# Performance work log

Hardware: AMD Instinct MI355X
Metric: run time of the kernel (lower is better)

Reference implementation:

```python
import jax, jax.numpy as jnp
import numpy as np

B, L, E, H, ENC, V, NL = 64, 512, 128, 512, 256, 4, 2
SOS = 4


def setup_inputs() -> dict:
    key = jax.random.key(0)
    ks = jax.random.split(key, 20)
    s = 0.05
    r = lambda k, shp: (jax.random.normal(k, shp, jnp.float32) * s)
    return {
        "encoder_outputs": jax.random.normal(ks[0], (B, L, ENC), jnp.float32),
        "targets": jax.random.randint(ks[1], (B, L), 0, V),
        "encoder_mask": jnp.ones((B, L), bool),
        "teacher_forcing_ratio": 1,
        "emb": r(ks[2], (V + 2, E)),
        "Wh": r(ks[3], (H, H)),
        "Ws": r(ks[4], (H, ENC)),
        "v": r(ks[5], (1, H)),
        "Wih0": r(ks[6], (3 * H, E + ENC)),
        "Whh0": r(ks[7], (3 * H, H)),
        "bih0": r(ks[8], (3 * H,)),
        "bhh0": r(ks[9], (3 * H,)),
        "Wih1": r(ks[10], (3 * H, H)),
        "Whh1": r(ks[11], (3 * H, H)),
        "bih1": r(ks[12], (3 * H,)),
        "bhh1": r(ks[13], (3 * H,)),
        "Wout": r(ks[14], (V, H)),
        "bout": r(ks[15], (V,)),
        "Winit": r(ks[16], (H * NL, ENC)),
        "binit": r(ks[17], (H * NL,)),
    }


def gru_cell(x, h, Wih, Whh, bih, bhh):
    # PyTorch GRUCell math
    gi = x @ Wih.T + bih
    gh = h @ Whh.T + bhh
    ir, iz, inn = jnp.split(gi, 3, axis=-1)
    hr, hz, hn = jnp.split(gh, 3, axis=-1)
    rg = jax.nn.sigmoid(ir + hr)
    zg = jax.nn.sigmoid(iz + hz)
    ng = jnp.tanh(inn + rg * hn)
    return (1.0 - zg) * ng + zg * h


def reference(encoder_outputs, targets, encoder_mask, teacher_forcing_ratio,
              emb, Wh, Ws, v, Wih0, Whh0, bih0, bhh0, Wih1, Whh1, bih1, bhh1,
              Wout, bout, Winit, binit):
    # init hidden: masked mean-pool -> linear -> tanh, (NL, B, H)
    maskf = encoder_mask[..., None].astype(jnp.float32)
    pooled = (encoder_outputs * maskf).sum(1) / jnp.clip(maskf.sum(1), 1.0)
    h0 = jnp.tanh((pooled @ Winit.T + binit).reshape(B, NL, H).transpose(1, 0, 2))

    # attention keys precomputed once (same linear applied each step in torch)
    keys = jnp.einsum('ble,he->blh', encoder_outputs, Ws)  # (B, L, H)

    # teacher forcing ratio fixed at 1 -> inputs known ahead of time
    tokens = jnp.concatenate([jnp.full((B, 1), SOS, targets.dtype), targets[:, :-1]], axis=1)
    emb_seq = emb[tokens]  # (B, L, E)

    neg = jnp.finfo(jnp.float32).min

    def step(h, e_t):
        q = h[-1] @ Wh.T                                   # (B, H)
        energy = jnp.tanh(q[:, None, :] + keys)            # (B, L, H)
        scores = jnp.einsum('blh,h->bl', energy, v[0])     # (B, L)
        scores = jnp.where(encoder_mask, scores, neg)
        attn = jax.nn.softmax(scores, axis=-1)
        ctx = jnp.einsum('bl,ble->be', attn, encoder_outputs)
        x = jnp.concatenate([e_t, ctx], axis=-1)           # (B, E+ENC)
        h0n = gru_cell(x, h[0], Wih0, Whh0, bih0, bhh0)
        h1n = gru_cell(h0n, h[1], Wih1, Whh1, bih1, bhh1)
        logits = h1n @ Wout.T + bout                       # (B, V)
        return jnp.stack([h0n, h1n]), logits

    _, logits = jax.lax.scan(step, h0, emb_seq.transpose(1, 0, 2))
    return logits.transpose(1, 0, 2)  # (B, L, V)
```

## Files before the change

kernel.cpp:

```cpp
#include <hip/hip_runtime.h>
#include <cstdint>
#include <cstddef>


#define BB   64
#define LL   512
#define EE   128
#define HH   512
#define ED   256
#define VV   4
#define SOS  4

#define NBLK 256
#define NTHR 512

typedef unsigned short ushort8 __attribute__((ext_vector_type(8)));
typedef unsigned int uint;

static const size_t OFF_KEYS = 0;
static const size_t OFF_WH   = 33554432;
static const size_t OFF_WHH0 = 34078720;
static const size_t OFF_WIH1 = 35651584;
static const size_t OFF_WHH1 = 37224448;
static const size_t OFF_WIHC = 38797312;
static const size_t OFF_GTOK = 39583744;
static const size_t OFF_H0   = 39620608;
static const size_t OFF_H1   = 39751680;
static const size_t OFF_QQ   = 39882752;
static const size_t OFF_CTXP = 40407040;
static const size_t OFF_SS   = 40669184;
static const size_t OFF_H0Q  = 40670208;
static const size_t OFF_H1Q  = 40801280;
static const size_t OFF_FLG  = 40932352;
static const size_t OFF_CNT  = 40948736;
static const size_t OFF_LP   = 40949248;

#define L_KEYS 0
#define L_H0F  131072
#define L_H1F  133120
#define L_Q    135168
#define L_VV   137344
#define L_CTX  139520
#define L_SCB  140544
#define L_ATB  141056
#define L_CT   141568
#define L_RED  142592
#define L_PRED 142656
#define L_GH0  154944
#define L_GH1  156480
#define L_TOT  158016

__device__ __forceinline__ int qidx(int h) { return h + ((h >> 7) << 3); }

__device__ __forceinline__ float bfu(unsigned short u) {
  return __uint_as_float(((unsigned)u) << 16);
}
__device__ __forceinline__ float bflo(uint u) { return __uint_as_float(u << 16); }
__device__ __forceinline__ float bfhi(uint u) { return __uint_as_float(u & 0xffff0000u); }
__device__ __forceinline__ unsigned short f2bf(float f) {
  unsigned u = __float_as_uint(f);
  unsigned r = 0x7FFFu + ((u >> 16) & 1u);
  return (unsigned short)((u + r) >> 16);
}
__device__ __forceinline__ float tanh_fast(float x) {
  x = __builtin_amdgcn_fmed3f(x, -10.f, 10.f);
  float t = __builtin_amdgcn_exp2f(x * 2.8853900817779268f);
  return (t - 1.f) * __builtin_amdgcn_rcpf(t + 1.f);
}
__device__ __forceinline__ float sigmoid_fast(float x) {
  x = __builtin_amdgcn_fmed3f(x, -30.f, 30.f);
  float t = __builtin_amdgcn_exp2f(x * -1.4426950408889634f);
  return __builtin_amdgcn_rcpf(1.f + t);
}
__device__ __forceinline__ float exp_fast(float x) {
  return __builtin_amdgcn_exp2f(x * 1.4426950408889634f);
}
__device__ __forceinline__ float gloadf(const float* p) {
  return __hip_atomic_load(p, __ATOMIC_RELAXED, __HIP_MEMORY_SCOPE_AGENT);
}
__device__ __forceinline__ void gstoref(float* p, float v) {
  __hip_atomic_store(p, v, __ATOMIC_RELAXED, __HIP_MEMORY_SCOPE_AGENT);
}
__device__ __forceinline__ uint gloadu(const uint* p) {
  return __hip_atomic_load(p, __ATOMIC_RELAXED, __HIP_MEMORY_SCOPE_AGENT);
}
__device__ __forceinline__ void gstoreu(uint* p, uint v) {
  __hip_atomic_store(p, v, __ATOMIC_RELAXED, __HIP_MEMORY_SCOPE_AGENT);
}

__device__ __forceinline__ void quad_sync(char* ws, int b, int j, uint gen) {
  asm volatile("s_waitcnt vmcnt(0)" ::: "memory");
  __syncthreads();
  if (threadIdx.x == 0) {
    uint* fl = (uint*)(ws + OFF_FLG);
    gstoreu(fl + (size_t)(b * 4 + j) * 16, gen);
    #pragma unroll
    for (int p = 0; p < 4; ++p) {
      if (p == j) continue;
      while (gloadu(fl + (size_t)(b * 4 + p) * 16) < gen)
        __builtin_amdgcn_s_sleep(4);
    }
  }
  __syncthreads();
}


__global__ void k_prep(const float* Wh, const float* Whh0, const float* Wih0,
                       const float* Wih1, const float* Whh1, char* ws) {
  unsigned short* Whbf   = (unsigned short*)(ws + OFF_WH);
  unsigned short* Whh0bf = (unsigned short*)(ws + OFF_WHH0);
  unsigned short* Wih1bf = (unsigned short*)(ws + OFF_WIH1);
  unsigned short* Whh1bf = (unsigned short*)(ws + OFF_WHH1);
  unsigned short* WihCbf = (unsigned short*)(ws + OFF_WIHC);
  const int tot = 262144 + 786432 * 3 + 393216;
  for (int i = blockIdx.x * blockDim.x + threadIdx.x; i < tot; i += gridDim.x * blockDim.x) {
    if (i < 262144) { Whbf[i] = f2bf(Wh[i]); }
    else if (i < 262144 + 786432) { int jj = i - 262144; Whh0bf[jj] = f2bf(Whh0[jj]); }
    else if (i < 262144 + 2 * 786432) { int jj = i - 262144 - 786432; Wih1bf[jj] = f2bf(Wih1[jj]); }
    else if (i < 262144 + 3 * 786432) { int jj = i - 262144 - 2 * 786432; Whh1bf[jj] = f2bf(Whh1[jj]); }
    else {
      int jj = i - 262144 - 3 * 786432;
      int r = jj >> 8, e = jj & 255;
      WihCbf[jj] = f2bf(Wih0[(size_t)r * 384 + 128 + e]);
    }
  }
}

__global__ void k_gitok(const float* emb, const float* Wih0, const float* bih0, char* ws) {
  float* gt = (float*)(ws + OFF_GTOK);
  const int vt = blockIdx.x;
  const int tid = threadIdx.x;
  __shared__ float ev[EE];
  if (tid < EE) ev[tid] = emb[(size_t)vt * EE + tid];
  __syncthreads();
  for (int r = tid; r < 1536; r += 256) {
    float a = bih0[r];
    const float* wr = Wih0 + (size_t)r * 384;
    for (int e = 0; e < EE; ++e) a += wr[e] * ev[e];
    gt[(size_t)vt * 1536 + r] = a;
  }
}

__global__ void k_keys(const float* enc, const float* Ws, char* ws) {
  unsigned short* keys = (unsigned short*)(ws + OFF_KEYS);
  __shared__ float et[32][ED];
  const int tid = threadIdx.x;
  const int row0 = blockIdx.x * 32;
  for (int r = 0; r < 32; ++r) et[r][tid] = enc[(size_t)(row0 + r) * ED + tid];
  __syncthreads();
  for (int hhh = 0; hhh < 2; ++hhh) {
    const int h = hhh * 256 + tid;
    float acc[32];
    #pragma unroll
    for (int ll = 0; ll < 32; ++ll) acc[ll] = 0.f;
    const float4* wrow = (const float4*)(Ws + (size_t)h * ED);
    for (int e4 = 0; e4 < 64; ++e4) {
      float4 w = wrow[e4];
      #pragma unroll
      for (int ll = 0; ll < 32; ++ll) {
        acc[ll] += w.x * et[ll][e4 * 4] + w.y * et[ll][e4 * 4 + 1]
                 + w.z * et[ll][e4 * 4 + 2] + w.w * et[ll][e4 * 4 + 3];
      }
    }
    for (int ll = 0; ll < 32; ++ll)
      keys[(size_t)(row0 + ll) * HH + h] = f2bf(acc[ll]);
  }
}

__global__ void k_init(const float* enc, const float* Winit, const float* binit, char* ws) {
  const int b = blockIdx.x;
  const int tid = threadIdx.x;
  __shared__ float pooled[ED];
  float acc = 0.f;
  for (int l = 0; l < LL; ++l) acc += enc[((size_t)b * LL + l) * ED + tid];
  pooled[tid] = acc * (1.0f / 512.0f);
  __syncthreads();
  float* h0 = (float*)(ws + OFF_H0);
  float* h1 = (float*)(ws + OFF_H1);
  for (int pass = 0; pass < 4; ++pass) {
    const int jj = pass * 256 + tid;
    float a = binit[jj];
    const float* wr = Winit + (size_t)jj * ED;
    for (int e = 0; e < ED; ++e) a += wr[e] * pooled[e];
    const float val = tanh_fast(a);
    const int nl = jj >> 9, h = jj & 511;
    if (nl == 0) h0[(size_t)b * HH + h] = val;
    else h1[(size_t)b * HH + h] = val;
  }
  if (b == 0) {
    uint* fl = (uint*)(ws + OFF_FLG);
    for (int i = tid; i < 4096; i += 256) fl[i] = 0u;
    uint* cnt = (uint*)(ws + OFF_CNT);
    if (tid < 128) cnt[tid] = 0u;
  }
}

__launch_bounds__(NTHR, 1)
__global__ void k_decode(char* ws, const float* enc, const int* targets,
                         const float* vvec, const float* bhh0, const float* bhh1,
                         const float* bih1, const float* Wout) {
  extern __shared__ char smem[];
  const int tid = threadIdx.x;

  __shared__ int roleSh[2];
  if (tid == 0) {
    uint xcd;
    asm volatile("s_getreg_b32 %0, hwreg(HW_REG_XCC_ID)" : "=s"(xcd));
    xcd &= 7u;
    uint* cnt = (uint*)(ws + OFF_CNT);
    uint rank = __hip_atomic_fetch_add(cnt + (size_t)xcd * 16, 1u,
                                       __ATOMIC_RELAXED, __HIP_MEMORY_SCOPE_AGENT);
    roleSh[0] = (int)((((xcd >> 2) * 32) + rank) & 63);
    roleSh[1] = (int)(xcd & 3);
  }
  __syncthreads();
  const int b = roleSh[0], j = roleSh[1];

  const unsigned short* keysg  = (const unsigned short*)(ws + OFF_KEYS);
  const unsigned short* Whbf   = (const unsigned short*)(ws + OFF_WH);
  const unsigned short* Whh0bf = (const unsigned short*)(ws + OFF_WHH0);
  const unsigned short* Wih1bf = (const unsigned short*)(ws + OFF_WIH1);
  const unsigned short* Whh1bf = (const unsigned short*)(ws + OFF_WHH1);
  const unsigned short* WihCbf = (const unsigned short*)(ws + OFF_WIHC);
  const float* gi_tok = (const float*)(ws + OFF_GTOK);

  float* QQgf   = (float*)(ws + OFF_QQ)   + (size_t)b * 2048;
  float* CTXPgf = (float*)(ws + OFF_CTXP) + (size_t)b * 1024;
  float* SSg    = (float*)(ws + OFF_SS)   + (size_t)b * 4;
  float* H0Qgf  = (float*)(ws + OFF_H0Q)  + (size_t)b * 512;
  float* H1Qgf  = (float*)(ws + OFF_H1Q)  + (size_t)b * 512;
  float* lp     = (float*)(ws + OFF_LP);

  float* h0f  = (float*)(smem + L_H0F);
  float* h1f  = (float*)(smem + L_H1F);
  float* qb   = (float*)(smem + L_Q);
  float* vvl  = (float*)(smem + L_VV);
  float* ctx  = (float*)(smem + L_CTX);
  float* scb  = (float*)(smem + L_SCB);
  float* atb  = (float*)(smem + L_ATB);
  float* ctmp = (float*)(smem + L_CT);
  float* wred = (float*)(smem + L_RED);
  float* pRed = (float*)(smem + L_PRED);
  float* gh0own = (float*)(smem + L_GH0);
  float* gh1own = (float*)(smem + L_GH1);

  const int r7 = tid & 127, seg = tid >> 7;

  for (int idx = tid; idx < 8192; idx += NTHR) {
    const int l = idx >> 6, hs = idx & 63;
    ushort8 kv = *(const ushort8*)(keysg + ((size_t)(b * LL + j * 128 + l) * HH + hs * 8));
    *(ushort8*)(smem + L_KEYS + l * 1024 + ((hs * 16) ^ ((l & 7) << 4))) = kv;
  }
  vvl[qidx(tid)] = vvec[tid];
  h0f[tid] = ((const float*)(ws + OFF_H0))[(size_t)b * HH + tid];
  h1f[tid] = ((const float*)(ws + OFF_H1))[(size_t)b * HH + tid];

  uint encp[32];
  {
    const int e = tid >> 1, lh = tid & 1;
    const float* ebase = enc + ((size_t)(b * LL + j * 128 + lh * 64)) * ED + e;
    #pragma unroll
    for (int jj = 0; jj < 32; ++jj) {
      float a0 = ebase[(size_t)(2 * jj) * ED];
      float a1 = ebase[(size_t)(2 * jj + 1) * ED];
      encp[jj] = (uint)f2bf(a0) | ((uint)f2bf(a1) << 16);
    }
  }
  uint whq[64];
  #pragma unroll
  for (int i = 0; i < 64; ++i)
    whq[i] = *(const uint*)(Whbf + (size_t)tid * HH + j * 128 + i * 2);

  __syncthreads();

  {
    float qr = 0.f;
    #pragma unroll 16
    for (int i = 0; i < 64; ++i)
      qr += bflo(whq[i]) * h1f[j * 128 + 2 * i] + bfhi(whq[i]) * h1f[j * 128 + 2 * i + 1];
    gstoref(QQgf + (size_t)j * 512 + tid, qr);
    if (tid < 128) gstoref(H1Qgf + (size_t)j * 128 + tid, h1f[j * 128 + tid]);
    quad_sync(ws, b, j, 1u);
  }

  for (int t = 0; t < LL; ++t) {
    {
      if (tid < 384) {
        const int ps = tid >> 7, i = tid & 127;
        const int p = ps + (ps >= j);
        h1f[p * 128 + i] = gloadf(H1Qgf + (size_t)p * 128 + i);
      }
      {
        float qv = gloadf(QQgf + 0 * 512 + tid) + gloadf(QQgf + 1 * 512 + tid)
                 + gloadf(QQgf + 2 * 512 + tid) + gloadf(QQgf + 3 * 512 + tid);
        qb[qidx(tid)] = qv;
      }
      __syncthreads();

      {
        float acc[6] = {0.f, 0.f, 0.f, 0.f, 0.f, 0.f};
        const int ks = seg * 128;
        #pragma unroll
        for (int g = 0; g < 3; ++g) {
          const ushort8* w0 = (const ushort8*)(Whh0bf + (size_t)(g * 512 + j * 128 + r7) * 512 + ks);
          const ushort8* w1 = (const ushort8*)(Whh1bf + (size_t)(g * 512 + j * 128 + r7) * 512 + ks);
          for (int k8 = 0; k8 < 16; ++k8) {
            ushort8 a8 = w0[k8];
            ushort8 b8 = w1[k8];
            #pragma unroll
            for (int u = 0; u < 8; ++u) {
              const float h0v = h0f[ks + k8 * 8 + u];
              const float h1v = h1f[ks + k8 * 8 + u];
              acc[g]     += bfu(a8[u]) * h0v;
              acc[3 + g] += bfu(b8[u]) * h1v;
            }
          }
        }
        #pragma unroll
        for (int u = 0; u < 6; ++u) pRed[(seg * 6 + u) * 128 + r7] = acc[u];
      }

      {
        const int lloc = tid >> 2, hq = tid & 3;
        const char* kbase = smem + L_KEYS + lloc * 1024;
        const int xo = (lloc & 7) << 4;
        const float* qh = qb + hq * 136;
        const float* vh = vvl + hq * 136;
        float s = 0.f;
        #pragma unroll 4
        for (int i8 = 0; i8 < 16; ++i8) {
          ushort8 kk = *(const ushort8*)(kbase + ((hq * 256 + i8 * 16) ^ xo));
          #pragma unroll
          for (int u = 0; u < 8; ++u)
            s += vh[i8 * 8 + u] * tanh_fast(qh[i8 * 8 + u] + bfu(kk[u]));
        }
        s += __shfl_xor(s, 1);
        s += __shfl_xor(s, 2);
        if (hq == 0) scb[lloc] = s;
      }
      __syncthreads();

      {
        float e = 0.f;
        if (tid < 128) { e = exp_fast(scb[tid]); atb[tid] = e; }
        float s2 = e;
        #pragma unroll
        for (int off = 32; off >= 1; off >>= 1) s2 += __shfl_xor(s2, off);
        if ((tid & 63) == 0 && tid < 128) wred[tid >> 6] = s2;
      }
      __syncthreads();

      {
        const int e = tid >> 1, lh = tid & 1;
        const float* atp = atb + lh * 64;
        float a = 0.f;
        #pragma unroll
        for (int jj = 0; jj < 32; ++jj) {
          uint u = encp[jj];
          a += atp[2 * jj] * bflo(u) + atp[2 * jj + 1] * bfhi(u);
        }
        a += __shfl_xor(a, 1);
        if (lh == 0) ctmp[e] = a;
      }
      if (tid < 384) {
        const int g = tid >> 7, r = tid & 127;
        gh0own[g * 128 + r] = pRed[(0 * 6 + g) * 128 + r] + pRed[(1 * 6 + g) * 128 + r]
                            + pRed[(2 * 6 + g) * 128 + r] + pRed[(3 * 6 + g) * 128 + r]
                            + bhh0[g * 512 + j * 128 + r];
        gh1own[g * 128 + r] = pRed[(0 * 6 + 3 + g) * 128 + r] + pRed[(1 * 6 + 3 + g) * 128 + r]
                            + pRed[(2 * 6 + 3 + g) * 128 + r] + pRed[(3 * 6 + 3 + g) * 128 + r]
                            + bhh1[g * 512 + j * 128 + r];
      }
      __syncthreads();

      if (tid < 256) gstoref(CTXPgf + (size_t)j * 256 + tid, ctmp[tid]);
      if (tid == 0) gstoref(SSg + j, wred[0] + wred[1]);
    }
    quad_sync(ws, b, j, (uint)(3 * t + 2));

    {
      if (tid < 256) {
        float S4 = gloadf(SSg + 0) + gloadf(SSg + 1) + gloadf(SSg + 2) + gloadf(SSg + 3);
        const float rS = __builtin_amdgcn_rcpf(S4);
        ctx[tid] = (gloadf(CTXPgf + 0 * 256 + tid) + gloadf(CTXPgf + 1 * 256 + tid)
                  + gloadf(CTXPgf + 2 * 256 + tid) + gloadf(CTXPgf + 3 * 256 + tid)) * rS;
      }
      __syncthreads();
      {
        float acc[3] = {0.f, 0.f, 0.f};
        const int ks = seg * 64;
        #pragma unroll
        for (int g = 0; g < 3; ++g) {
          const ushort8* w = (const ushort8*)(WihCbf + (size_t)(g * 512 + j * 128 + r7) * 256 + ks);
          for (int k8 = 0; k8 < 8; ++k8) {
            ushort8 a8 = w[k8];
            #pragma unroll
            for (int u = 0; u < 8; ++u)
              acc[g] += bfu(a8[u]) * ctx[ks + k8 * 8 + u];
          }
        }
        #pragma unroll
        for (int g = 0; g < 3; ++g) pRed[(seg * 6 + g) * 128 + r7] = acc[g];
      }
      __syncthreads();
      if (tid < 128) {
        const int r = tid;
        const int tok = (t == 0) ? SOS : targets[(size_t)b * LL + t - 1];
        const float* gt = gi_tok + (size_t)tok * 1536 + j * 128 + r;
        float gi[3];
        #pragma unroll
        for (int g = 0; g < 3; ++g)
          gi[g] = pRed[(0 * 6 + g) * 128 + r] + pRed[(1 * 6 + g) * 128 + r]
                + pRed[(2 * 6 + g) * 128 + r] + pRed[(3 * 6 + g) * 128 + r]
                + gt[g * 512];
        const float rg = sigmoid_fast(gi[0] + gh0own[0 * 128 + r]);
        const float zg = sigmoid_fast(gi[1] + gh0own[1 * 128 + r]);
        const float ng = tanh_fast(gi[2] + rg * gh0own[2 * 128 + r]);
        h0f[j * 128 + r] = (1.f - zg) * ng + zg * h0f[j * 128 + r];
      }
      __syncthreads();
      if (tid < 128) gstoref(H0Qgf + (size_t)j * 128 + tid, h0f[j * 128 + tid]);
    }
    quad_sync(ws, b, j, (uint)(3 * t + 3));

    if (tid < 384) {
      const int ps = tid >> 7, i = tid & 127;
      const int p = ps + (ps >= j);
      h0f[p * 128 + i] = gloadf(H0Qgf + (size_t)p * 128 + i);
    }
    __syncthreads();

    {
      {
        float acc[3] = {0.f, 0.f, 0.f};
        const int ks = seg * 128;
        #pragma unroll
        for (int g = 0; g < 3; ++g) {
          const ushort8* w = (const ushort8*)(Wih1bf + (size_t)(g * 512 + j * 128 + r7) * 512 + ks);
          for (int k8 = 0; k8 < 16; ++k8) {
            ushort8 a8 = w[k8];
            #pragma unroll
            for (int u = 0; u < 8; ++u)
              acc[g] += bfu(a8[u]) * h0f[ks + k8 * 8 + u];
          }
        }
        #pragma unroll
        for (int g = 0; g < 3; ++g) pRed[(seg * 6 + g) * 128 + r7] = acc[g];
      }
      __syncthreads();
      if (tid < 128) {
        const int r = tid;
        float gi[3];
        #pragma unroll
        for (int g = 0; g < 3; ++g)
          gi[g] = pRed[(0 * 6 + g) * 128 + r] + pRed[(1 * 6 + g) * 128 + r]
                + pRed[(2 * 6 + g) * 128 + r] + pRed[(3 * 6 + g) * 128 + r]
                + bih1[g * 512 + j * 128 + r];
        const float rg = sigmoid_fast(gi[0] + gh1own[0 * 128 + r]);
        const float zg = sigmoid_fast(gi[1] + gh1own[1 * 128 + r]);
        const float ng = tanh_fast(gi[2] + rg * gh1own[2 * 128 + r]);
        h1f[j * 128 + r] = (1.f - zg) * ng + zg * h1f[j * 128 + r];
      }
      __syncthreads();
      {
        float qr = 0.f;
        #pragma unroll 16
        for (int i = 0; i < 64; ++i)
          qr += bflo(whq[i]) * h1f[j * 128 + 2 * i] + bfhi(whq[i]) * h1f[j * 128 + 2 * i + 1];
        gstoref(QQgf + (size_t)j * 512 + tid, qr);
      }
      if (tid < 128) gstoref(H1Qgf + (size_t)j * 128 + tid, h1f[j * 128 + tid]);
      if (tid >= 128 && tid < 256) {
        const int g = tid - 128;
        const int v = g >> 5, i = g & 31;
        float a = 0.f;
        #pragma unroll
        for (int k = 0; k < 4; ++k)
          a += Wout[(size_t)v * HH + j * 128 + i * 4 + k] * h1f[j * 128 + i * 4 + k];
        a += __shfl_xor(a, 16); a += __shfl_xor(a, 8);
        a += __shfl_xor(a, 4);  a += __shfl_xor(a, 2); a += __shfl_xor(a, 1);
        if (i == 0) lp[((size_t)t * BB + b) * 16 + j * 4 + v] = a;
      }
    }
    quad_sync(ws, b, j, (uint)(3 * t + 4));
  }
}

__global__ void k_lsum(const char* ws, const float* bout, float* out) {
  const float* lp = (const float*)(ws + OFF_LP);
  const int i = blockIdx.x * 256 + threadIdx.x;
  if (i >= BB * LL * VV) return;
  const int v = i & 3, t = (i >> 2) & 511, b = i >> 11;
  float a = bout[v];
  #pragma unroll
  for (int jj = 0; jj < 4; ++jj)
    a += lp[((size_t)t * BB + b) * 16 + jj * 4 + v];
  out[i] = a;
}

extern "C" void kernel_launch(void* const* d_in, const int* in_sizes, int n_in,
                              void* d_out, int out_size, void* d_ws, size_t ws_size,
                              hipStream_t stream) {
  char* ws = (char*)d_ws;
  const float* enc     = (const float*)d_in[0];
  const int*   targets = (const int*)d_in[1];
  const float* emb   = (const float*)d_in[4];
  const float* Wh    = (const float*)d_in[5];
  const float* Ws    = (const float*)d_in[6];
  const float* vvec  = (const float*)d_in[7];
  const float* Wih0  = (const float*)d_in[8];
  const float* Whh0  = (const float*)d_in[9];
  const float* bih0  = (const float*)d_in[10];
  const float* bhh0  = (const float*)d_in[11];
  const float* Wih1  = (const float*)d_in[12];
  const float* Whh1  = (const float*)d_in[13];
  const float* bih1  = (const float*)d_in[14];
  const float* bhh1  = (const float*)d_in[15];
  const float* Wout  = (const float*)d_in[16];
  const float* bout  = (const float*)d_in[17];
  const float* Winit = (const float*)d_in[18];
  const float* binit = (const float*)d_in[19];

  k_prep <<<1024, 256, 0, stream>>>(Wh, Whh0, Wih0, Wih1, Whh1, ws);
  k_gitok<<<6,    256, 0, stream>>>(emb, Wih0, bih0, ws);
  k_keys <<<1024, 256, 0, stream>>>(enc, Ws, ws);
  k_init <<<64,   256, 0, stream>>>(enc, Winit, binit, ws);

  (void)hipFuncSetAttribute((const void*)k_decode,
                            hipFuncAttributeMaxDynamicSharedMemorySize, L_TOT);

  {
    void* kws = (void*)ws;
    void* ken = (void*)enc;
    void* ktg = (void*)targets;
    void* kvv = (void*)vvec;
    void* kb0 = (void*)bhh0;
    void* kb1 = (void*)bhh1;
    void* kbi = (void*)bih1;
    void* kwo = (void*)Wout;
    void* args[] = { &kws, &ken, &ktg, &kvv, &kb0, &kb1, &kbi, &kwo };
    hipError_t ce = hipLaunchCooperativeKernel((const void*)k_decode, dim3(NBLK), dim3(NTHR),
                                               args, L_TOT, stream);
    if (ce != hipSuccess) {
      k_decode<<<dim3(NBLK), dim3(NTHR), L_TOT, stream>>>(ws, enc, targets, vvec,
                                                          bhh0, bhh1, bih1, Wout);
    }
  }

  k_lsum<<<512, 256, 0, stream>>>(ws, bout, (float*)d_out);
}
```

Measured before the change: 54.01 ms.

## Split each batch row across eight blocks and exchange hidden state as bf16

Each batch element's decode is now split across 8 blocks (one per XCD) of 256 threads instead of 4 blocks of 512. Each block owns 64 hidden units and 64 encoder positions, and two blocks are allowed per CU. Hidden state, query partials and the shared h vectors are packed as bf16 pairs to halve inter-block exchange traffic. The 8-way flag barrier polls peers in parallel from 8 threads. This spreads the per-step work over more CUs and cuts per-block work, at the cost of more synchronization participants and lower precision in the exchanged state.

```diff
diff --git a/kernel.cpp b/kernel.cpp
--- a/kernel.cpp
+++ b/kernel.cpp
@@ -11,8 +11,8 @@
 #define VV   4
 #define SOS  4
 
-#define NBLK 256
-#define NTHR 512
+#define NBLK 512
+#define NTHR 256
 
 typedef unsigned short ushort8 __attribute__((ext_vector_type(8)));
 typedef unsigned int uint;
@@ -28,29 +28,28 @@
 static const size_t OFF_H1   = 39751680;
 static const size_t OFF_QQ   = 39882752;
 static const size_t OFF_CTXP = 40407040;
-static const size_t OFF_SS   = 40669184;
-static const size_t OFF_H0Q  = 40670208;
-static const size_t OFF_H1Q  = 40801280;
-static const size_t OFF_FLG  = 40932352;
-static const size_t OFF_CNT  = 40948736;
-static const size_t OFF_LP   = 40949248;
+static const size_t OFF_SS   = 40931328;
+static const size_t OFF_H0Q  = 40933376;
+static const size_t OFF_H1Q  = 40998912;
+static const size_t OFF_FLG  = 41064448;
+static const size_t OFF_CNT  = 41097216;
+static const size_t OFF_LP   = 41097728;
 
 #define L_KEYS 0
-#define L_H0F  131072
-#define L_H1F  133120
-#define L_Q    135168
-#define L_VV   137344
-#define L_CTX  139520
-#define L_SCB  140544
-#define L_ATB  141056
-#define L_CT   141568
-#define L_RED  142592
-#define L_PRED 142656
-#define L_GH0  154944
-#define L_GH1  156480
-#define L_TOT  158016
-
-__device__ __forceinline__ int qidx(int h) { return h + ((h >> 7) << 3); }
+#define L_H0F  65536
+#define L_H1F  66560
+#define L_QB   67584
+#define L_VV   69696
+#define L_CTX  71808
+#define L_SCB  72832
+#define L_ATB  73088
+#define L_RED  73344
+#define L_PRED 73408
+#define L_GH0  76480
+#define L_GH1  77248
+#define L_H0O  78016
+#define L_H1O  78272
+#define L_TOT  78528
 
 __device__ __forceinline__ float bfu(unsigned short u) {
   return __uint_as_float(((unsigned)u) << 16);
@@ -62,6 +61,9 @@
   unsigned r = 0x7FFFu + ((u >> 16) & 1u);
   return (unsigned short)((u + r) >> 16);
 }
+__device__ __forceinline__ uint packbf(float a, float b) {
+  return (uint)f2bf(a) | ((uint)f2bf(b) << 16);
+}
 __device__ __forceinline__ float tanh_fast(float x) {
   x = __builtin_amdgcn_fmed3f(x, -10.f, 10.f);
   float t = __builtin_amdgcn_exp2f(x * 2.8853900817779268f);
@@ -88,18 +90,16 @@
   __hip_atomic_store(p, v, __ATOMIC_RELAXED, __HIP_MEMORY_SCOPE_AGENT);
 }
 
-__device__ __forceinline__ void quad_sync(char* ws, int b, int j, uint gen) {
+__device__ __forceinline__ void octet_sync(char* ws, int b, int j, uint gen) {
   asm volatile("s_waitcnt vmcnt(0)" ::: "memory");
   __syncthreads();
-  if (threadIdx.x == 0) {
-    uint* fl = (uint*)(ws + OFF_FLG);
-    gstoreu(fl + (size_t)(b * 4 + j) * 16, gen);
-    #pragma unroll
-    for (int p = 0; p < 4; ++p) {
-      if (p == j) continue;
-      while (gloadu(fl + (size_t)(b * 4 + p) * 16) < gen)
-        __builtin_amdgcn_s_sleep(4);
-    }
+  const int tid = threadIdx.x;
+  uint* fl = (uint*)(ws + OFF_FLG);
+  if (tid == 0)
+    gstoreu(fl + (size_t)(b * 8 + j) * 16, gen);
+  if (tid < 8 && tid != j) {
+    while (gloadu(fl + (size_t)(b * 8 + tid) * 16) < gen)
+      __builtin_amdgcn_s_sleep(4);
   }
   __syncthreads();
 }
@@ -189,13 +189,13 @@
   }
   if (b == 0) {
     uint* fl = (uint*)(ws + OFF_FLG);
-    for (int i = tid; i < 4096; i += 256) fl[i] = 0u;
+    for (int i = tid; i < 8192; i += 256) fl[i] = 0u;
     uint* cnt = (uint*)(ws + OFF_CNT);
     if (tid < 128) cnt[tid] = 0u;
   }
 }
 
-__launch_bounds__(NTHR, 1)
+__launch_bounds__(NTHR, 2)
 __global__ void k_decode(char* ws, const float* enc, const int* targets,
                          const float* vvec, const float* bhh0, const float* bhh1,
                          const float* bih1, const float* Wout) {
@@ -210,8 +210,8 @@
     uint* cnt = (uint*)(ws + OFF_CNT);
     uint rank = __hip_atomic_fetch_add(cnt + (size_t)xcd * 16, 1u,
                                        __ATOMIC_RELAXED, __HIP_MEMORY_SCOPE_AGENT);
-    roleSh[0] = (int)((((xcd >> 2) * 32) + rank) & 63);
-    roleSh[1] = (int)(xcd & 3);
+    roleSh[0] = (int)(rank & 63);
+    roleSh[1] = (int)xcd;
   }
   __syncthreads();
   const int b = roleSh[0], j = roleSh[1];
@@ -224,265 +224,297 @@
   const unsigned short* WihCbf = (const unsigned short*)(ws + OFF_WIHC);
   const float* gi_tok = (const float*)(ws + OFF_GTOK);
 
-  float* QQgf   = (float*)(ws + OFF_QQ)   + (size_t)b * 2048;
-  float* CTXPgf = (float*)(ws + OFF_CTXP) + (size_t)b * 1024;
-  float* SSg    = (float*)(ws + OFF_SS)   + (size_t)b * 4;
-  float* H0Qgf  = (float*)(ws + OFF_H0Q)  + (size_t)b * 512;
-  float* H1Qgf  = (float*)(ws + OFF_H1Q)  + (size_t)b * 512;
-  float* lp     = (float*)(ws + OFF_LP);
-
-  float* h0f  = (float*)(smem + L_H0F);
-  float* h1f  = (float*)(smem + L_H1F);
-  float* qb   = (float*)(smem + L_Q);
-  float* vvl  = (float*)(smem + L_VV);
-  float* ctx  = (float*)(smem + L_CTX);
-  float* scb  = (float*)(smem + L_SCB);
-  float* atb  = (float*)(smem + L_ATB);
-  float* ctmp = (float*)(smem + L_CT);
-  float* wred = (float*)(smem + L_RED);
-  float* pRed = (float*)(smem + L_PRED);
+  uint*  QQg   = (uint*)(ws + OFF_QQ)   + (size_t)b * 2048;
+  float* CTXPg = (float*)(ws + OFF_CTXP) + (size_t)b * 2048;
+  float* SSg   = (float*)(ws + OFF_SS)  + (size_t)b * 8;
+  uint*  H0Qg  = (uint*)(ws + OFF_H0Q)  + (size_t)b * 256;
+  uint*  H1Qg  = (uint*)(ws + OFF_H1Q)  + (size_t)b * 256;
+  float* lp    = (float*)(ws + OFF_LP);
+
+  uint*  h0u   = (uint*)(smem + L_H0F);
+  uint*  h1u   = (uint*)(smem + L_H1F);
+  float* qbf   = (float*)(smem + L_QB);
+  float* vvf   = (float*)(smem + L_VV);
+  float* ctx   = (float*)(smem + L_CTX);
+  float* scb   = (float*)(smem + L_SCB);
+  float* atb   = (float*)(smem + L_ATB);
+  float* wred  = (float*)(smem + L_RED);
+  float* pRed  = (float*)(smem + L_PRED);
   float* gh0own = (float*)(smem + L_GH0);
   float* gh1own = (float*)(smem + L_GH1);
-
-  const int r7 = tid & 127, seg = tid >> 7;
-
-  for (int idx = tid; idx < 8192; idx += NTHR) {
-    const int l = idx >> 6, hs = idx & 63;
-    ushort8 kv = *(const ushort8*)(keysg + ((size_t)(b * LL + j * 128 + l) * HH + hs * 8));
+  float* h0own = (float*)(smem + L_H0O);
+  float* h1own = (float*)(smem + L_H1O);
+
+  for (int c = tid; c < 4096; c += NTHR) {
+    const int l = c >> 6, hs = c & 63;
+    ushort8 kv = *(const ushort8*)(keysg + ((size_t)(b * LL + j * 64 + l) * HH + hs * 8));
     *(ushort8*)(smem + L_KEYS + l * 1024 + ((hs * 16) ^ ((l & 7) << 4))) = kv;
   }
-  vvl[qidx(tid)] = vvec[tid];
-  h0f[tid] = ((const float*)(ws + OFF_H0))[(size_t)b * HH + tid];
-  h1f[tid] = ((const float*)(ws + OFF_H1))[(size_t)b * HH + tid];
-
+  for (int h = tid; h < 512; h += NTHR)
+    vvf[(h >> 7) * 132 + (h & 127)] = vvec[h];
+  {
+    const float* H0g = (const float*)(ws + OFF_H0) + (size_t)b * HH;
+    const float* H1g = (const float*)(ws + OFF_H1) + (size_t)b * HH;
+    h0u[tid] = packbf(H0g[2 * tid], H0g[2 * tid + 1]);
+    h1u[tid] = packbf(H1g[2 * tid], H1g[2 * tid + 1]);
+    if (tid < 64) {
+      h0own[tid] = H0g[j * 64 + tid];
+      h1own[tid] = H1g[j * 64 + tid];
+    }
+  }
   uint encp[32];
   {
-    const int e = tid >> 1, lh = tid & 1;
-    const float* ebase = enc + ((size_t)(b * LL + j * 128 + lh * 64)) * ED + e;
+    const float* ebase = enc + ((size_t)(b * LL + j * 64)) * ED + tid;
     #pragma unroll
-    for (int jj = 0; jj < 32; ++jj) {
-      float a0 = ebase[(size_t)(2 * jj) * ED];
-      float a1 = ebase[(size_t)(2 * jj + 1) * ED];
-      encp[jj] = (uint)f2bf(a0) | ((uint)f2bf(a1) << 16);
-    }
+    for (int k = 0; k < 32; ++k)
+      encp[k] = packbf(ebase[(size_t)(2 * k) * ED], ebase[(size_t)(2 * k + 1) * ED]);
   }
   uint whq[64];
   #pragma unroll
-  for (int i = 0; i < 64; ++i)
-    whq[i] = *(const uint*)(Whbf + (size_t)tid * HH + j * 128 + i * 2);
-
+  for (int i = 0; i < 32; ++i) {
+    whq[i]      = *(const uint*)(Whbf + (size_t)(2 * tid) * HH + j * 64 + 2 * i);
+    whq[32 + i] = *(const uint*)(Whbf + (size_t)(2 * tid + 1) * HH + j * 64 + 2 * i);
+  }
   __syncthreads();
 
   {
-    float qr = 0.f;
-    #pragma unroll 16
-    for (int i = 0; i < 64; ++i)
-      qr += bflo(whq[i]) * h1f[j * 128 + 2 * i] + bfhi(whq[i]) * h1f[j * 128 + 2 * i + 1];
-    gstoref(QQgf + (size_t)j * 512 + tid, qr);
-    if (tid < 128) gstoref(H1Qgf + (size_t)j * 128 + tid, h1f[j * 128 + tid]);
-    quad_sync(ws, b, j, 1u);
-  }
+    float q0 = 0.f, q1 = 0.f;
+    #pragma unroll
+    for (int i = 0; i < 32; ++i) {
+      const float hl = h1own[2 * i], hh = h1own[2 * i + 1];
+      q0 += bflo(whq[i]) * hl + bfhi(whq[i]) * hh;
+      q1 += bflo(whq[32 + i]) * hl + bfhi(whq[32 + i]) * hh;
+    }
+    gstoreu(QQg + (size_t)j * 256 + tid, packbf(q0, q1));
+    if (tid < 32) gstoreu(H1Qg + (size_t)j * 32 + tid,
+                          packbf(h1own[2 * tid], h1own[2 * tid + 1]));
+  }
+  octet_sync(ws, b, j, 1u);
 
   for (int t = 0; t < LL; ++t) {
     {
-      if (tid < 384) {
-        const int ps = tid >> 7, i = tid & 127;
+      float qlo = 0.f, qhi = 0.f;
+      #pragma unroll
+      for (int p = 0; p < 8; ++p) {
+        uint u = gloadu(QQg + (size_t)p * 256 + tid);
+        qlo += bflo(u); qhi += bfhi(u);
+      }
+      const int hq = tid >> 6, i2 = (tid & 63) * 2;
+      qbf[hq * 132 + i2] = qlo;
+      qbf[hq * 132 + i2 + 1] = qhi;
+      if (tid < 224) {
+        const int ps = tid >> 5, i = tid & 31;
         const int p = ps + (ps >= j);
-        h1f[p * 128 + i] = gloadf(H1Qgf + (size_t)p * 128 + i);
-      }
-      {
-        float qv = gloadf(QQgf + 0 * 512 + tid) + gloadf(QQgf + 1 * 512 + tid)
-                 + gloadf(QQgf + 2 * 512 + tid) + gloadf(QQgf + 3 * 512 + tid);
-        qb[qidx(tid)] = qv;
-      }
+        h1u[p * 32 + i] = gloadu(H1Qg + (size_t)p * 32 + i);
+      }
+    }
+    __syncthreads();
+
+    {
+      const int mat = tid >> 7, seg = (tid >> 6) & 1, r = tid & 63;
+      const unsigned short* W = mat ? Whh1bf : Whh0bf;
+      const uint* hsrc = (mat ? h1u : h0u) + seg * 128;
+      const ushort8* w0 = (const ushort8*)(W + (size_t)(0 * 512 + j * 64 + r) * 512 + seg * 256);
+      const ushort8* w1 = (const ushort8*)(W + (size_t)(1 * 512 + j * 64 + r) * 512 + seg * 256);
+      const ushort8* w2 = (const ushort8*)(W + (size_t)(2 * 512 + j * 64 + r) * 512 + seg * 256);
+      float a0 = 0.f, a1 = 0.f, a2 = 0.f;
+      for (int k8 = 0; k8 < 32; ++k8) {
+        const uint4 hu = *(const uint4*)(hsrc + k8 * 4);
+        const ushort8 u0 = w0[k8], u1 = w1[k8], u2 = w2[k8];
+        float hv[8];
+        hv[0] = bflo(hu.x); hv[1] = bfhi(hu.x); hv[2] = bflo(hu.y); hv[3] = bfhi(hu.y);
+        hv[4] = bflo(hu.z); hv[5] = bfhi(hu.z); hv[6] = bflo(hu.w); hv[7] = bfhi(hu.w);
+        #pragma unroll
+        for (int u = 0; u < 8; ++u) {
+          a0 += bfu(u0[u]) * hv[u];
+          a1 += bfu(u1[u]) * hv[u];
+          a2 += bfu(u2[u]) * hv[u];
+        }
+      }
+      pRed[((mat * 2 + seg) * 3 + 0) * 64 + r] = a0;
+      pRed[((mat * 2 + seg) * 3 + 1) * 64 + r] = a1;
+      pRed[((mat * 2 + seg) * 3 + 2) * 64 + r] = a2;
+    }
+
+    {
+      const int lloc = tid >> 2, hq = tid & 3;
+      const char* kbase = smem + L_KEYS + lloc * 1024;
+      const int xo = (lloc & 7) << 4;
+      const float* qh = qbf + hq * 132;
+      const float* vh = vvf + hq * 132;
+      float s = 0.f;
+      for (int i8 = 0; i8 < 16; ++i8) {
+        ushort8 kk = *(const ushort8*)(kbase + ((hq * 256 + i8 * 16) ^ xo));
+        const float* q8 = qh + i8 * 8;
+        const float* v8 = vh + i8 * 8;
+        #pragma unroll
+        for (int u = 0; u < 8; ++u)
+          s += v8[u] * tanh_fast(q8[u] + bfu(kk[u]));
+      }
+      s += __shfl_xor(s, 1);
+      s += __shfl_xor(s, 2);
+      if (hq == 0) scb[lloc] = s;
+    }
+    __syncthreads();
+
+    if (tid < 64) {
+      float e = exp_fast(scb[tid]);
+      atb[tid] = e;
+      float s2 = e;
+      #pragma unroll
+      for (int off = 32; off >= 1; off >>= 1) s2 += __shfl_xor(s2, off);
+      if (tid == 0) gstoref(SSg + j, s2);
+    }
+    __syncthreads();
+
+    {
+      float a = 0.f;
+      #pragma unroll
+      for (int k = 0; k < 32; ++k) {
+        uint u = encp[k];
+        a += atb[2 * k] * bflo(u) + atb[2 * k + 1] * bfhi(u);
+      }
+      gstoref(CTXPg + (size_t)j * 256 + tid, a);
+    }
+    for (int o = tid; o < 384; o += NTHR) {
+      const int m = (o >= 192) ? 1 : 0, oo = o - m * 192, g = oo >> 6, r = oo & 63;
+      const float v = pRed[((m * 2 + 0) * 3 + g) * 64 + r]
+                    + pRed[((m * 2 + 1) * 3 + g) * 64 + r]
+                    + (m ? bhh1 : bhh0)[g * 512 + j * 64 + r];
+      (m ? gh1own : gh0own)[g * 64 + r] = v;
+    }
+    octet_sync(ws, b, j, (uint)(3 * t + 2));
+
+    {
+      float cp0 = gloadf(CTXPg + 0 * 256 + tid), cp1 = gloadf(CTXPg + 1 * 256 + tid);
+      float cp2 = gloadf(CTXPg + 2 * 256 + tid), cp3 = gloadf(CTXPg + 3 * 256 + tid);
+      float cp4 = gloadf(CTXPg + 4 * 256 + tid), cp5 = gloadf(CTXPg + 5 * 256 + tid);
+      float cp6 = gloadf(CTXPg + 6 * 256 + tid), cp7 = gloadf(CTXPg + 7 * 256 + tid);
+      if (tid < 8) wred[tid] = gloadf(SSg + tid);
       __syncthreads();
-
-      {
-        float acc[6] = {0.f, 0.f, 0.f, 0.f, 0.f, 0.f};
-        const int ks = seg * 128;
+      const float S8 = ((wred[0] + wred[1]) + (wred[2] + wred[3]))
+                     + ((wred[4] + wred[5]) + (wred[6] + wred[7]));
+      const float rS = __builtin_amdgcn_rcpf(S8);
+      ctx[tid] = (((cp0 + cp1) + (cp2 + cp3)) + ((cp4 + cp5) + (cp6 + cp7))) * rS;
+    }
+    __syncthreads();
+    {
+      const int r = tid & 63, q4 = tid >> 6;
+      const ushort8* w0 = (const ushort8*)(WihCbf + (size_t)(0 * 512 + j * 64 + r) * 256 + q4 * 64);
+      const ushort8* w1 = (const ushort8*)(WihCbf + (size_t)(1 * 512 + j * 64 + r) * 256 + q4 * 64);
+      const ushort8* w2 = (const ushort8*)(WihCbf + (size_t)(2 * 512 + j * 64 + r) * 256 + q4 * 64);
+      const float* cx = ctx + q4 * 64;
+      float a0 = 0.f, a1 = 0.f, a2 = 0.f;
+      for (int k8 = 0; k8 < 8; ++k8) {
+        const ushort8 u0 = w0[k8], u1 = w1[k8], u2 = w2[k8];
         #pragma unroll
-        for (int g = 0; g < 3; ++g) {
-          const ushort8* w0 = (const ushort8*)(Whh0bf + (size_t)(g * 512 + j * 128 + r7) * 512 + ks);
-          const ushort8* w1 = (const ushort8*)(Whh1bf + (size_t)(g * 512 + j * 128 + r7) * 512 + ks);
-          for (int k8 = 0; k8 < 16; ++k8) {
-            ushort8 a8 = w0[k8];
-            ushort8 b8 = w1[k8];
-            #pragma unroll
-            for (int u = 0; u < 8; ++u) {
-              const float h0v = h0f[ks + k8 * 8 + u];
-              const float h1v = h1f[ks + k8 * 8 + u];
-              acc[g]     += bfu(a8[u]) * h0v;
-              acc[3 + g] += bfu(b8[u]) * h1v;
-            }
-          }
+        for (int u = 0; u < 8; ++u) {
+          const float c = cx[k8 * 8 + u];
+          a0 += bfu(u0[u]) * c; a1 += bfu(u1[u]) * c; a2 += bfu(u2[u]) * c;
         }
+      }
+      pRed[(q4 * 3 + 0) * 64 + r] = a0;
+      pRed[(q4 * 3 + 1) * 64 + r] = a1;
+      pRed[(q4 * 3 + 2) * 64 + r] = a2;
+    }
+    __syncthreads();
+    if (tid < 64) {
+      const int r = tid;
+      const int tok = (t == 0) ? SOS : targets[(size_t)b * LL + t - 1];
+      const float* gt = gi_tok + (size_t)tok * 1536 + j * 64 + r;
+      const float g0 = pRed[(0 * 3 + 0) * 64 + r] + pRed[(1 * 3 + 0) * 64 + r]
+                     + pRed[(2 * 3 + 0) * 64 + r] + pRed[(3 * 3 + 0) * 64 + r] + gt[0];
+      const float g1 = pRed[(0 * 3 + 1) * 64 + r] + pRed[(1 * 3 + 1) * 64 + r]
+                     + pRed[(2 * 3 + 1) * 64 + r] + pRed[(3 * 3 + 1) * 64 + r] + gt[512];
+      const float g2 = pRed[(0 * 3 + 2) * 64 + r] + pRed[(1 * 3 + 2) * 64 + r]
+                     + pRed[(2 * 3 + 2) * 64 + r] + pRed[(3 * 3 + 2) * 64 + r] + gt[1024];
+      const float rg = sigmoid_fast(g0 + gh0own[r]);
+      const float zg = sigmoid_fast(g1 + gh0own[64 + r]);
+      const float ng = tanh_fast(g2 + rg * gh0own[128 + r]);
+      h0own[r] = (1.f - zg) * ng + zg * h0own[r];
+    }
+    __syncthreads();
+    if (tid < 32) {
+      const uint pk = packbf(h0own[2 * tid], h0own[2 * tid + 1]);
+      h0u[j * 32 + tid] = pk;
+      gstoreu(H0Qg + (size_t)j * 32 + tid, pk);
+    }
+    octet_sync(ws, b, j, (uint)(3 * t + 3));
+
+    if (tid < 224) {
+      const int ps = tid >> 5, i = tid & 31;
+      const int p = ps + (ps >= j);
+      h0u[p * 32 + i] = gloadu(H0Qg + (size_t)p * 32 + i);
+    }
+    __syncthreads();
+    {
+      const int r = tid & 63, s4 = tid >> 6;
+      const ushort8* w0 = (const ushort8*)(Wih1bf + (size_t)(0 * 512 + j * 64 + r) * 512 + s4 * 128);
+      const ushort8* w1 = (const ushort8*)(Wih1bf + (size_t)(1 * 512 + j * 64 + r) * 512 + s4 * 128);
+      const ushort8* w2 = (const ushort8*)(Wih1bf + (size_t)(2 * 512 + j * 64 + r) * 512 + s4 * 128);
+      const uint* hsrc = h0u + s4 * 64;
+      float a0 = 0.f, a1 = 0.f, a2 = 0.f;
+      for (int k8 = 0; k8 < 16; ++k8) {
+        const uint4 hu = *(const uint4*)(hsrc + k8 * 4);
+        const ushort8 u0 = w0[k8], u1 = w1[k8], u2 = w2[k8];
+        float hv[8];
+        hv[0] = bflo(hu.x); hv[1] = bfhi(hu.x); hv[2] = bflo(hu.y); hv[3] = bfhi(hu.y);
+        hv[4] = bflo(hu.z); hv[5] = bfhi(hu.z); hv[6] = bflo(hu.w); hv[7] = bfhi(hu.w);
         #pragma unroll
-        for (int u = 0; u < 6; ++u) pRed[(seg * 6 + u) * 128 + r7] = acc[u];
-      }
-
-      {
-        const int lloc = tid >> 2, hq = tid & 3;
-        const char* kbase = smem + L_KEYS + lloc * 1024;
-        const int xo = (lloc & 7) << 4;
-        const float* qh = qb + hq * 136;
-        const float* vh = vvl + hq * 136;
-        float s = 0.f;
-        #pragma unroll 4
-        for (int i8 = 0; i8 < 16; ++i8) {
-          ushort8 kk = *(const ushort8*)(kbase + ((hq * 256 + i8 * 16) ^ xo));
-          #pragma unroll
-          for (int u = 0; u < 8; ++u)
-            s += vh[i8 * 8 + u] * tanh_fast(qh[i8 * 8 + u] + bfu(kk[u]));
+        for (int u = 0; u < 8; ++u) {
+          a0 += bfu(u0[u]) * hv[u];
+          a1 += bfu(u1[u]) * hv[u];
+          a2 += bfu(u2[u]) * hv[u];
         }
-        s += __shfl_xor(s, 1);
-        s += __shfl_xor(s, 2);
-        if (hq == 0) scb[lloc] = s;
-      }
-      __syncthreads();
-
-      {
-        float e = 0.f;
-        if (tid < 128) { e = exp_fast(scb[tid]); atb[tid] = e; }
-        float s2 = e;
-        #pragma unroll
-        for (int off = 32; off >= 1; off >>= 1) s2 += __shfl_xor(s2, off);
-        if ((tid & 63) == 0 && tid < 128) wred[tid >> 6] = s2;
-      }
-      __syncthreads();
-
-      {
-        const int e = tid >> 1, lh = tid & 1;
-        const float* atp = atb + lh * 64;
-        float a = 0.f;
-        #pragma unroll
-        for (int jj = 0; jj < 32; ++jj) {
-          uint u = encp[jj];
-          a += atp[2 * jj] * bflo(u) + atp[2 * jj + 1] * bfhi(u);
-        }
-        a += __shfl_xor(a, 1);
-        if (lh == 0) ctmp[e] = a;
-      }
-      if (tid < 384) {
-        const int g = tid >> 7, r = tid & 127;
-        gh0own[g * 128 + r] = pRed[(0 * 6 + g) * 128 + r] + pRed[(1 * 6 + g) * 128 + r]
-                            + pRed[(2 * 6 + g) * 128 + r] + pRed[(3 * 6 + g) * 128 + r]
-                            + bhh0[g * 512 + j * 128 + r];
-        gh1own[g * 128 + r] = pRed[(0 * 6 + 3 + g) * 128 + r] + pRed[(1 * 6 + 3 + g) * 128 + r]
-                            + pRed[(2 * 6 + 3 + g) * 128 + r] + pRed[(3 * 6 + 3 + g) * 128 + r]
-                            + bhh1[g * 512 + j * 128 + r];
-      }
-      __syncthreads();
-
-      if (tid < 256) gstoref(CTXPgf + (size_t)j * 256 + tid, ctmp[tid]);
-      if (tid == 0) gstoref(SSg + j, wred[0] + wred[1]);
-    }
-    quad_sync(ws, b, j, (uint)(3 * t + 2));
-
-    {
-      if (tid < 256) {
-        float S4 = gloadf(SSg + 0) + gloadf(SSg + 1) + gloadf(SSg + 2) + gloadf(SSg + 3);
-        const float rS = __builtin_amdgcn_rcpf(S4);
-        ctx[tid] = (gloadf(CTXPgf + 0 * 256 + tid) + gloadf(CTXPgf + 1 * 256 + tid)
-                  + gloadf(CTXPgf + 2 * 256 + tid) + gloadf(CTXPgf + 3 * 256 + tid)) * rS;
-      }
-      __syncthreads();
-      {
-        float acc[3] = {0.f, 0.f, 0.f};
-        const int ks = seg * 64;
-        #pragma unroll
-        for (int g = 0; g < 3; ++g) {
-          const ushort8* w = (const ushort8*)(WihCbf + (size_t)(g * 512 + j * 128 + r7) * 256 + ks);
-          for (int k8 = 0; k8 < 8; ++k8) {
-            ushort8 a8 = w[k8];
-            #pragma unroll
-            for (int u = 0; u < 8; ++u)
-              acc[g] += bfu(a8[u]) * ctx[ks + k8 * 8 + u];
-          }
-        }
-        #pragma unroll
-        for (int g = 0; g < 3; ++g) pRed[(seg * 6 + g) * 128 + r7] = acc[g];
-      }
-      __syncthreads();
-      if (tid < 128) {
-        const int r = tid;
-        const int tok = (t == 0) ? SOS : targets[(size_t)b * LL + t - 1];
-        const float* gt = gi_tok + (size_t)tok * 1536 + j * 128 + r;
-        float gi[3];
-        #pragma unroll
-        for (int g = 0; g < 3; ++g)
-          gi[g] = pRed[(0 * 6 + g) * 128 + r] + pRed[(1 * 6 + g) * 128 + r]
-                + pRed[(2 * 6 + g) * 128 + r] + pRed[(3 * 6 + g) * 128 + r]
-                + gt[g * 512];
-        const float rg = sigmoid_fast(gi[0] + gh0own[0 * 128 + r]);
-        const float zg = sigmoid_fast(gi[1] + gh0own[1 * 128 + r]);
-        const float ng = tanh_fast(gi[2] + rg * gh0own[2 * 128 + r]);
-        h0f[j * 128 + r] = (1.f - zg) * ng + zg * h0f[j * 128 + r];
-      }
-      __syncthreads();
-      if (tid < 128) gstoref(H0Qgf + (size_t)j * 128 + tid, h0f[j * 128 + tid]);
-    }
-    quad_sync(ws, b, j, (uint)(3 * t + 3));
-
-    if (tid < 384) {
-      const int ps = tid >> 7, i = tid & 127;
-      const int p = ps + (ps >= j);
-      h0f[p * 128 + i] = gloadf(H0Qgf + (size_t)p * 128 + i);
-    }
-    __syncthreads();
-
-    {
-      {
-        float acc[3] = {0.f, 0.f, 0.f};
-        const int ks = seg * 128;
-        #pragma unroll
-        for (int g = 0; g < 3; ++g) {
-          const ushort8* w = (const ushort8*)(Wih1bf + (size_t)(g * 512 + j * 128 + r7) * 512 + ks);
-          for (int k8 = 0; k8 < 16; ++k8) {
-            ushort8 a8 = w[k8];
-            #pragma unroll
-            for (int u = 0; u < 8; ++u)
-              acc[g] += bfu(a8[u]) * h0f[ks + k8 * 8 + u];
-          }
-        }
-        #pragma unroll
-        for (int g = 0; g < 3; ++g) pRed[(seg * 6 + g) * 128 + r7] = acc[g];
-      }
-      __syncthreads();
-      if (tid < 128) {
-        const int r = tid;
-        float gi[3];
-        #pragma unroll
-        for (int g = 0; g < 3; ++g)
-          gi[g] = pRed[(0 * 6 + g) * 128 + r] + pRed[(1 * 6 + g) * 128 + r]
-                + pRed[(2 * 6 + g) * 128 + r] + pRed[(3 * 6 + g) * 128 + r]
-                + bih1[g * 512 + j * 128 + r];
-        const float rg = sigmoid_fast(gi[0] + gh1own[0 * 128 + r]);
-        const float zg = sigmoid_fast(gi[1] + gh1own[1 * 128 + r]);
-        const float ng = tanh_fast(gi[2] + rg * gh1own[2 * 128 + r]);
-        h1f[j * 128 + r] = (1.f - zg) * ng + zg * h1f[j * 128 + r];
-      }
-      __syncthreads();
-      {
-        float qr = 0.f;
-        #pragma unroll 16
-        for (int i = 0; i < 64; ++i)
-          qr += bflo(whq[i]) * h1f[j * 128 + 2 * i] + bfhi(whq[i]) * h1f[j * 128 + 2 * i + 1];
-        gstoref(QQgf + (size_t)j * 512 + tid, qr);
-      }
-      if (tid < 128) gstoref(H1Qgf + (size_t)j * 128 + tid, h1f[j * 128 + tid]);
-      if (tid >= 128 && tid < 256) {
-        const int g = tid - 128;
-        const int v = g >> 5, i = g & 31;
-        float a = 0.f;
-        #pragma unroll
-        for (int k = 0; k < 4; ++k)
-          a += Wout[(size_t)v * HH + j * 128 + i * 4 + k] * h1f[j * 128 + i * 4 + k];
-        a += __shfl_xor(a, 16); a += __shfl_xor(a, 8);
-        a += __shfl_xor(a, 4);  a += __shfl_xor(a, 2); a += __shfl_xor(a, 1);
-        if (i == 0) lp[((size_t)t * BB + b) * 16 + j * 4 + v] = a;
-      }
-    }
-    quad_sync(ws, b, j, (uint)(3 * t + 4));
+      }
+      pRed[(s4 * 3 + 0) * 64 + r] = a0;
+      pRed[(s4 * 3 + 1) * 64 + r] = a1;
+      pRed[(s4 * 3 + 2) * 64 + r] = a2;
+    }
+    __syncthreads();
+    if (tid < 64) {
+      const int r = tid;
+      const float g0 = pRed[(0 * 3 + 0) * 64 + r] + pRed[(1 * 3 + 0) * 64 + r]
+                     + pRed[(2 * 3 + 0) * 64 + r] + pRed[(3 * 3 + 0) * 64 + r]
+                     + bih1[0 * 512 + j * 64 + r];
+      const float g1 = pRed[(0 * 3 + 1) * 64 + r] + pRed[(1 * 3 + 1) * 64 + r]
+                     + pRed[(2 * 3 + 1) * 64 + r] + pRed[(3 * 3 + 1) * 64 + r]
+                     + bih1[1 * 512 + j * 64 + r];
+      const float g2 = pRed[(0 * 3 + 2) * 64 + r] + pRed[(1 * 3 + 2) * 64 + r]
+                     + pRed[(2 * 3 + 2) * 64 + r] + pRed[(3 * 3 + 2) * 64 + r]
+                     + bih1[2 * 512 + j * 64 + r];
+      const float rg = sigmoid_fast(g0 + gh1own[r]);
+      const float zg = sigmoid_fast(g1 + gh1own[64 + r]);
+      const float ng = tanh_fast(g2 + rg * gh1own[128 + r]);
+      h1own[r] = (1.f - zg) * ng + zg * h1own[r];
+    }
+    __syncthreads();
+    if (tid < 32) {
+      const uint pk = packbf(h1own[2 * tid], h1own[2 * tid + 1]);
+      h1u[j * 32 + tid] = pk;
+      gstoreu(H1Qg + (size_t)j * 32 + tid, pk);
+    }
+    {
+      float q0 = 0.f, q1 = 0.f;
+      #pragma unroll
+      for (int i = 0; i < 32; ++i) {
+        const float hl = h1own[2 * i], hh = h1own[2 * i + 1];
+        q0 += bflo(whq[i]) * hl + bfhi(whq[i]) * hh;
+        q1 += bflo(whq[32 + i]) * hl + bfhi(whq[32 + i]) * hh;
+      }
+      gstoreu(QQg + (size_t)j * 256 + tid, packbf(q0, q1));
+    }
+    if (tid >= 64 && tid < 128) {
+      const int lane = tid - 64, v = lane >> 4, i = lane & 15;
+      float a = 0.f;
+      #pragma unroll
+      for (int k = 0; k < 4; ++k)
+        a += Wout[(size_t)v * HH + j * 64 + i * 4 + k] * h1own[i * 4 + k];
+      a += __shfl_xor(a, 8); a += __shfl_xor(a, 4);
+      a += __shfl_xor(a, 2); a += __shfl_xor(a, 1);
+      if (i == 0) lp[(((size_t)t * BB + b) * 8 + j) * 4 + v] = a;
+    }
+    octet_sync(ws, b, j, (uint)(3 * t + 4));
   }
 }
 
@@ -493,8 +525,8 @@
   const int v = i & 3, t = (i >> 2) & 511, b = i >> 11;
   float a = bout[v];
   #pragma unroll
-  for (int jj = 0; jj < 4; ++jj)
-    a += lp[((size_t)t * BB + b) * 16 + jj * 4 + v];
+  for (int jj = 0; jj < 8; ++jj)
+    a += lp[(((size_t)t * BB + b) * 8 + jj) * 4 + v];
   out[i] = a;
 }
 
```

Result: faster. 49.90 ms (-7.6%).
